# Performance work log

Measured on AMD Instinct MI355X. Metric: run time of the kernel, lower is better.

The kernel has to match this reference:

```python
import jax, jax.numpy as jnp
import numpy as np

# Multi-scale feature pyramid (static: determines per-level slice bounds)
SPATIAL_SHAPES = np.array([[100, 100], [50, 50], [25, 25], [13, 13], [7, 7]])  # (H, W) per level
LEVEL_START = np.concatenate([[0], np.cumsum(SPATIAL_SHAPES[:, 0] * SPATIAL_SHAPES[:, 1])])[:-1]
C = 256       # hidden_inplanes
HEADS = 8     # head_nums
POINTS = 4    # point_nums
LEVELS = 5    # feature_level_nums
FF = 2048     # feedforward_planes
DH = C // HEADS


def setup_inputs() -> dict:
    key = jax.random.key(0)
    ks = jax.random.split(key, 16)
    B = 2
    L = int((SPATIAL_SHAPES[:, 0] * SPATIAL_SHAPES[:, 1]).sum())  # 13343 tokens
    s = 0.02
    return {
        'src': jax.random.normal(ks[0], (B, L, C), jnp.float32),
        'pos': jax.random.normal(ks[1], (B, L, C), jnp.float32) * 0.1,
        'reference_points': jax.random.uniform(ks[2], (B, L, LEVELS, 2), jnp.float32),
        'wv': jax.random.normal(ks[3], (C, C), jnp.float32) * s,
        'bv': jnp.zeros((C,), jnp.float32),
        'wo': jax.random.normal(ks[4], (C, HEADS * LEVELS * POINTS * 2), jnp.float32) * s,
        'bo': jax.random.normal(ks[5], (HEADS * LEVELS * POINTS * 2,), jnp.float32) * 0.5,
        'wa': jax.random.normal(ks[6], (C, HEADS * LEVELS * POINTS), jnp.float32) * s,
        'ba': jnp.zeros((HEADS * LEVELS * POINTS,), jnp.float32),
        'wout': jax.random.normal(ks[7], (C, C), jnp.float32) * s,
        'bout': jnp.zeros((C,), jnp.float32),
        'ln1g': jnp.ones((C,), jnp.float32),
        'ln1b': jnp.zeros((C,), jnp.float32),
        'w1': jax.random.normal(ks[8], (C, FF), jnp.float32) * s,
        'b1': jnp.zeros((FF,), jnp.float32),
        'w2': jax.random.normal(ks[9], (FF, C), jnp.float32) * s,
        'b2': jnp.zeros((C,), jnp.float32),
        'ln2g': jnp.ones((C,), jnp.float32),
        'ln2b': jnp.zeros((C,), jnp.float32),
    }


def layernorm(x, g, b, eps=1e-5):
    m = jnp.mean(x, -1, keepdims=True)
    v = jnp.var(x, -1, keepdims=True)
    return (x - m) * jax.lax.rsqrt(v + eps) * g + b


def bilinear_sample(val, loc, Hs, Ws):
    # val: [B, heads, H*W, dh]   loc: [B, heads, Lq, P, 2] normalized coords in [0,1]
    # grid_sample semantics, align_corners=False, zero padding outside
    px = loc[..., 0] * Ws - 0.5
    py = loc[..., 1] * Hs - 0.5
    x0 = jnp.floor(px); y0 = jnp.floor(py)
    lx = px - x0;       ly = py - y0
    x0i = x0.astype(jnp.int32); y0i = y0.astype(jnp.int32)
    gather = jax.vmap(jax.vmap(lambda v, i: v[i]))  # over batch, head dims
    out = jnp.zeros(loc.shape[:-1] + (val.shape[-1],), val.dtype)
    for dx, dy, w in ((0, 0, (1 - lx) * (1 - ly)), (1, 0, lx * (1 - ly)),
                      (0, 1, (1 - lx) * ly), (1, 1, lx * ly)):
        xi = x0i + dx; yi = y0i + dy
        valid = (xi >= 0) & (xi < Ws) & (yi >= 0) & (yi < Hs)
        idx = jnp.clip(yi, 0, Hs - 1) * Ws + jnp.clip(xi, 0, Ws - 1)
        g = gather(val, idx)  # [B, heads, Lq, P, dh]
        out = out + (w * valid)[..., None] * g
    return out


def msdeform_attn(query, value_in, ref, wv, bv, wo, bo, wa, ba, wout, bout):
    B, Lq, _ = query.shape
    # value projection -> [B, heads, Len, dh]
    value = (value_in @ wv + bv).reshape(B, -1, HEADS, DH).transpose(0, 2, 1, 3)
    offsets = (query @ wo + bo).reshape(B, Lq, HEADS, LEVELS, POINTS, 2)
    attn = jax.nn.softmax((query @ wa + ba).reshape(B, Lq, HEADS, LEVELS * POINTS), -1)
    attn = attn.reshape(B, Lq, HEADS, LEVELS, POINTS)
    # offset normalizer = (W, H) per level
    norml = jnp.asarray(SPATIAL_SHAPES[:, ::-1].copy(), jnp.float32)
    loc = ref[:, :, None, :, None, :] + offsets / norml[None, None, None, :, None, :]
    acc = jnp.zeros((B, Lq, HEADS, DH), query.dtype)
    for l in range(LEVELS):
        Hs, Ws = int(SPATIAL_SHAPES[l, 0]), int(SPATIAL_SHAPES[l, 1])
        s = int(LEVEL_START[l])
        vl = value[:, :, s:s + Hs * Ws, :]
        locl = jnp.transpose(loc[:, :, :, l], (0, 2, 1, 3, 4))  # [B, heads, Lq, P, 2]
        samp = bilinear_sample(vl, locl, Hs, Ws)                 # [B, heads, Lq, P, dh]
        acc = acc + jnp.einsum('bhqpd,bqhp->bqhd', samp, attn[:, :, :, l])
    return acc.reshape(B, Lq, C) @ wout + bout


def reference(src, pos, reference_points, wv, bv, wo, bo, wa, ba, wout, bout,
              ln1g, ln1b, w1, b1, w2, b2, ln2g, ln2b):
    # DeformableTransformerEncoderLayer (eval mode, dropout off)
    q = src + pos
    src2 = msdeform_attn(q, src, reference_points, wv, bv, wo, bo, wa, ba, wout, bout)
    x = layernorm(src + src2, ln1g, ln1b)
    ffn = jax.nn.relu(x @ w1 + b1) @ w2 + b2
    return layernorm(x + ffn, ln2g, ln2b)
```

## Files before the change

### kernel.cpp

```cpp
#include <hip/hip_runtime.h>
#include <hip/hip_bf16.h>
#include <hip/hip_fp16.h>

typedef __hip_bfloat16 bf16;
typedef unsigned short ushort_t;
typedef __attribute__((ext_vector_type(8))) short bf16x8;
typedef __attribute__((ext_vector_type(16))) float f32x16;

__device__ __forceinline__ float us2f(unsigned short u) {
    unsigned int x = ((unsigned int)u) << 16;
    return __uint_as_float(x);
}
__device__ __forceinline__ ushort_t f2us(float f) {
    return ((__hip_bfloat16_raw)__float2bfloat16(f)).x;
}

__device__ __forceinline__ void gl_lds16(const ushort_t* g, ushort_t* l) {
    __builtin_amdgcn_global_load_lds(
        (const __attribute__((address_space(1))) void*)g,
        (__attribute__((address_space(3))) void*)l, 16, 0, 0);
}

__global__ __launch_bounds__(256) void cast2_kernel(
    const float* __restrict__ src, const float* __restrict__ pos,
    bf16* __restrict__ src_b, bf16* __restrict__ q_b, int n)
{
    int i = (blockIdx.x * 256 + threadIdx.x) * 4;
    if (i < n) {
        const float4 s4 = *reinterpret_cast<const float4*>(&src[i]);
        const float4 p4 = *reinterpret_cast<const float4*>(&pos[i]);
        int2 sp, qp;
        sp.x = (unsigned)f2us(s4.x) | ((unsigned)f2us(s4.y) << 16);
        sp.y = (unsigned)f2us(s4.z) | ((unsigned)f2us(s4.w) << 16);
        qp.x = (unsigned)f2us(s4.x + p4.x) | ((unsigned)f2us(s4.y + p4.y) << 16);
        qp.y = (unsigned)f2us(s4.z + p4.z) | ((unsigned)f2us(s4.w + p4.w) << 16);
        *reinterpret_cast<int2*>((ushort_t*)src_b + i) = sp;
        *reinterpret_cast<int2*>((ushort_t*)q_b + i) = qp;
    }
}

__global__ __launch_bounds__(256) void prep_kernel(
    const float* __restrict__ wv, const float* __restrict__ wo,
    const float* __restrict__ wa, const float* __restrict__ wout,
    const float* __restrict__ w1, const float* __restrict__ w2,
    const float* __restrict__ bo, const float* __restrict__ ba,
    bf16* __restrict__ wvt, bf16* __restrict__ wcat, bf16* __restrict__ woutt,
    bf16* __restrict__ w1t, bf16* __restrict__ w2t, float* __restrict__ bcat)
{
    __shared__ float tile[32][33];
    const int b = blockIdx.x;
    const float* W; bf16* Wt; int K, N, tb;
    if (b < 64)        { W = wv;   Wt = wvt;            K = 256;  N = 256;  tb = b; }
    else if (b < 144)  { W = wo;   Wt = wcat;           K = 256;  N = 320;  tb = b - 64; }
    else if (b < 184)  { W = wa;   Wt = wcat + 320*256; K = 256;  N = 160;  tb = b - 144; }
    else if (b < 248)  { W = wout; Wt = woutt;          K = 256;  N = 256;  tb = b - 184; }
    else if (b < 760)  { W = w1;   Wt = w1t;            K = 256;  N = 2048; tb = b - 248; }
    else if (b < 1272) { W = w2;   Wt = w2t;            K = 2048; N = 256;  tb = b - 760; }
    else {
        int i = (b - 1272) * 256 + threadIdx.x;
        if (i < 320) bcat[i] = bo[i];
        else if (i < 480) bcat[i] = ba[i - 320];
        return;
    }
    const int ntn = N >> 5;
    const int nb = (tb % ntn) * 32, kb = (tb / ntn) * 32;
    const int tx = threadIdx.x & 31, ty = threadIdx.x >> 5;
    #pragma unroll
    for (int i = 0; i < 32; i += 8) {
        int k = kb + ty + i, n = nb + tx;
        tile[ty + i][tx] = (k < K && n < N) ? W[(size_t)k * N + n] : 0.f;
    }
    __syncthreads();
    #pragma unroll
    for (int i = 0; i < 32; i += 8) {
        int n = nb + ty + i, k = kb + tx;
        if (n < N && k < K)
            Wt[(size_t)n * K + k] = __float2bfloat16(tile[tx][ty + i]);
    }
}

template<bool RELU, bool OUT_BF16, bool HAS_RESID, bool RESID_BF16, int NT, int WPE>
__global__ __launch_bounds__(256, WPE) void gemm_mfma_s(
    const ushort_t* __restrict__ A,
    const ushort_t* __restrict__ Bt,
    const float* __restrict__ bias,
    const void* __restrict__ residv,
    void* __restrict__ outv, int M, int N, int K, int mtiles)
{
    __shared__ __align__(16) char smemraw[24576];
    ushort_t* Asmem = (ushort_t*)smemraw;
    ushort_t* Bsmem = (ushort_t*)(smemraw + 4096);
    float (*epi)[68] = (float(*)[68])smemraw;

    const int lid = blockIdx.x;
    const int tbk = lid >> 3;
    const int xb = tbk & (NT - 1);
    const int yg = (tbk / NT) * 8 + (lid & 7);
    if (yg >= mtiles) return;
    const int m0 = yg * 64;
    const int n0 = xb * 128;

    const int tid = threadIdx.x;
    const int lane = tid & 63;
    const int wave = tid >> 6;
    const int l32 = lane & 31;
    const int hi  = lane >> 5;
    const int wm = wave >> 1;
    const int wn = wave & 1;

    const int lsup = lane >> 3;
    const int clin = lane & 7;

    const int gsA = wave * 8 + lsup;
    const int csA = clin ^ (gsA & 7);
    int rA = m0 + gsA * 2 + (csA >> 2); if (rA > M - 1) rA = M - 1;
    const ushort_t* aP = A + (size_t)rA * K + (csA & 3) * 8;
    ushort_t* aL = Asmem + wave * 512;

    const ushort_t* bP[2]; ushort_t* bL[2];
    #pragma unroll
    for (int i = 0; i < 2; ++i) {
        const int gsB = wave * 16 + i * 8 + lsup;
        const int csB = clin ^ (gsB & 7);
        int rB = n0 + gsB * 2 + (csB >> 2); if (rB > N - 1) rB = N - 1;
        bP[i] = Bt + (size_t)rB * K + (csB & 3) * 8;
        bL[i] = Bsmem + (wave * 16 + i * 8) * 64;
    }

    const int arow = wm * 32 + l32;
    const int asup = arow >> 1;
    const ushort_t* aR[2];
    #pragma unroll
    for (int kw = 0; kw < 2; ++kw) {
        const int q = kw * 2 + hi;
        const int slot = (((arow & 1) << 2) | q) ^ (asup & 7);
        aR[kw] = Asmem + asup * 64 + slot * 8;
    }
    const ushort_t* bR[2][2];
    #pragma unroll
    for (int j = 0; j < 2; ++j) {
        const int brow = wn * 64 + j * 32 + l32;
        const int bsup = brow >> 1;
        #pragma unroll
        for (int kw = 0; kw < 2; ++kw) {
            const int q = kw * 2 + hi;
            const int slot = (((brow & 1) << 2) | q) ^ (bsup & 7);
            bR[j][kw] = Bsmem + bsup * 64 + slot * 8;
        }
    }

    f32x16 acc[2] = {};

    auto stage = [&](int ofs) {
        gl_lds16(aP, aL + ofs);             aP    += 32;
        gl_lds16(bP[0], bL[0] + ofs);       bP[0] += 32;
        gl_lds16(bP[1], bL[1] + ofs);       bP[1] += 32;
    };
    auto compute = [&](int ofs) {
        #pragma unroll
        for (int kw = 0; kw < 2; ++kw) {
            const bf16x8 af = *reinterpret_cast<const bf16x8*>(aR[kw] + ofs);
            #pragma unroll
            for (int j = 0; j < 2; ++j)
                acc[j] = __builtin_amdgcn_mfma_f32_32x32x16_bf16(
                    af, *reinterpret_cast<const bf16x8*>(bR[j][kw] + ofs),
                    acc[j], 0, 0, 0);
        }
    };

    const int ntile = K >> 5;
    stage(0);
    for (int t = 0; t < ntile; t += 2) {
        __syncthreads();
        stage(6144);
        compute(0);
        __syncthreads();
        if (t + 2 < ntile) stage(0);
        compute(6144);
    }
    __syncthreads();

    #pragma unroll
    for (int half = 0; half < 2; ++half) {
        if (wn == half) {
            #pragma unroll
            for (int j = 0; j < 2; ++j) {
                const int coll = j * 32 + l32;
                const int n = n0 + half * 64 + coll;
                const float bv = (n < N) ? bias[n] : 0.f;
                #pragma unroll
                for (int r = 0; r < 16; ++r) {
                    const int row = wm * 32 + hi * 4 + (r & 3) + (r >> 2) * 8;
                    epi[row][coll] = acc[j][r] + bv;
                }
            }
        }
        __syncthreads();
        #pragma unroll
        for (int i = 0; i < 4; ++i) {
            const int idx = i * 256 + tid;
            const int row = idx >> 4;
            const int c4  = idx & 15;
            const int m = m0 + row;
            const int n = n0 + half * 64 + c4 * 4;
            if (m < M && n + 3 < N) {
                float4 v = *reinterpret_cast<const float4*>(&epi[row][c4 * 4]);
                if (HAS_RESID) {
                    if (RESID_BF16) {
                        const int2 rw = *reinterpret_cast<const int2*>(
                            (const ushort_t*)residv + (size_t)m * N + n);
                        v.x += us2f((ushort_t)((unsigned)rw.x & 0xffffu));
                        v.y += us2f((ushort_t)((unsigned)rw.x >> 16));
                        v.z += us2f((ushort_t)((unsigned)rw.y & 0xffffu));
                        v.w += us2f((ushort_t)((unsigned)rw.y >> 16));
                    } else {
                        const float4 r4 = *reinterpret_cast<const float4*>(
                            (const float*)residv + (size_t)m * N + n);
                        v.x += r4.x; v.y += r4.y; v.z += r4.z; v.w += r4.w;
                    }
                }
                if (RELU) {
                    v.x = fmaxf(v.x, 0.f); v.y = fmaxf(v.y, 0.f);
                    v.z = fmaxf(v.z, 0.f); v.w = fmaxf(v.w, 0.f);
                }
                if (OUT_BF16) {
                    int2 pk;
                    pk.x = (unsigned)f2us(v.x) | ((unsigned)f2us(v.y) << 16);
                    pk.y = (unsigned)f2us(v.z) | ((unsigned)f2us(v.w) << 16);
                    *reinterpret_cast<int2*>((ushort_t*)outv + (size_t)m * N + n) = pk;
                } else {
                    *reinterpret_cast<float4*>((float*)outv + (size_t)m * N + n) = v;
                }
            }
        }
        if (half == 0) __syncthreads();
    }
}

template<bool RELU, bool OUT_BF16, bool HAS_RESID, bool RESID_BF16, int NT>
__global__ __launch_bounds__(256, 4) void gemm_mfma_b(
    const ushort_t* __restrict__ A,
    const ushort_t* __restrict__ Bt,
    const float* __restrict__ bias,
    const void* __restrict__ residv,
    void* __restrict__ outv, int M, int N, int K, int mtiles)
{
    __shared__ __align__(16) char smemraw[32768];
    ushort_t* Asmem = (ushort_t*)smemraw;
    ushort_t* Bsmem = (ushort_t*)(smemraw + 8192);
    float (*epi)[68] = (float(*)[68])smemraw;

    const int lid = blockIdx.x;
    const int tbk = lid >> 3;
    const int xb = tbk & (NT - 1);
    const int yg = (tbk / NT) * 8 + (lid & 7);
    if (yg >= mtiles) return;
    const int m0 = yg * 128;
    const int n0 = xb * 128;

    const int tid = threadIdx.x;
    const int lane = tid & 63;
    const int wave = tid >> 6;
    const int l32 = lane & 31;
    const int hi  = lane >> 5;
    const int wm = wave >> 1;
    const int wn = wave & 1;

    const int lsup = lane >> 3;
    const int clin = lane & 7;
    const ushort_t *aP[2], *bP[2];
    ushort_t *aL[2], *bL[2];
    #pragma unroll
    for (int i = 0; i < 2; ++i) {
        const int gs = wave * 16 + i * 8 + lsup;
        const int cs = clin ^ (gs & 7);
        int rA = m0 + gs * 2 + (cs >> 2); if (rA > M - 1) rA = M - 1;
        aP[i] = A + (size_t)rA * K + (cs & 3) * 8;
        aL[i] = Asmem + (wave * 16 + i * 8) * 64;
        int rB = n0 + gs * 2 + (cs >> 2); if (rB > N - 1) rB = N - 1;
        bP[i] = Bt + (size_t)rB * K + (cs & 3) * 8;
        bL[i] = Bsmem + (wave * 16 + i * 8) * 64;
    }

    const ushort_t* aR[2][2];
    const ushort_t* bR[2][2];
    #pragma unroll
    for (int mi = 0; mi < 2; ++mi) {
        const int arow = wm * 64 + mi * 32 + l32;
        const int asup = arow >> 1;
        #pragma unroll
        for (int kw = 0; kw < 2; ++kw) {
            const int q = kw * 2 + hi;
            const int slot = (((arow & 1) << 2) | q) ^ (asup & 7);
            aR[mi][kw] = Asmem + asup * 64 + slot * 8;
        }
    }
    #pragma unroll
    for (int ni = 0; ni < 2; ++ni) {
        const int brow = wn * 64 + ni * 32 + l32;
        const int bsup = brow >> 1;
        #pragma unroll
        for (int kw = 0; kw < 2; ++kw) {
            const int q = kw * 2 + hi;
            const int slot = (((brow & 1) << 2) | q) ^ (bsup & 7);
            bR[ni][kw] = Bsmem + bsup * 64 + slot * 8;
        }
    }

    f32x16 a00 = {}, a01 = {}, a10 = {}, a11 = {};

    auto stage = [&](int ofs) {
        gl_lds16(aP[0], aL[0] + ofs); aP[0] += 32;
        gl_lds16(aP[1], aL[1] + ofs); aP[1] += 32;
        gl_lds16(bP[0], bL[0] + ofs); bP[0] += 32;
        gl_lds16(bP[1], bL[1] + ofs); bP[1] += 32;
    };
    auto compute = [&](int ofs) {
        #pragma unroll
        for (int kw = 0; kw < 2; ++kw) {
            const bf16x8 af0 = *reinterpret_cast<const bf16x8*>(aR[0][kw] + ofs);
            const bf16x8 af1 = *reinterpret_cast<const bf16x8*>(aR[1][kw] + ofs);
            const bf16x8 bf0 = *reinterpret_cast<const bf16x8*>(bR[0][kw] + ofs);
            const bf16x8 bf1 = *reinterpret_cast<const bf16x8*>(bR[1][kw] + ofs);
            a00 = __builtin_amdgcn_mfma_f32_32x32x16_bf16(af0, bf0, a00, 0, 0, 0);
            a01 = __builtin_amdgcn_mfma_f32_32x32x16_bf16(af0, bf1, a01, 0, 0, 0);
            a10 = __builtin_amdgcn_mfma_f32_32x32x16_bf16(af1, bf0, a10, 0, 0, 0);
            a11 = __builtin_amdgcn_mfma_f32_32x32x16_bf16(af1, bf1, a11, 0, 0, 0);
        }
    };

    const int ntile = K >> 5;
    stage(0);
    for (int t = 0; t < ntile; t += 2) {
        __syncthreads();
        stage(8192);
        compute(0);
        __syncthreads();
        if (t + 2 < ntile) stage(0);
        compute(8192);
    }
    __syncthreads();

    #pragma unroll
    for (int qd = 0; qd < 4; ++qd) {
        const int rh = qd >> 1, ch = qd & 1;
        if (qd) __syncthreads();
        if (wm == rh && wn == ch) {
            #pragma unroll
            for (int ni = 0; ni < 2; ++ni) {
                const int col = ni * 32 + l32;
                const int n = n0 + ch * 64 + col;
                const float bv = (n < N) ? bias[n] : 0.f;
                #pragma unroll
                for (int mi = 0; mi < 2; ++mi) {
                    const f32x16& ac = (mi == 0) ? (ni == 0 ? a00 : a01)
                                                 : (ni == 0 ? a10 : a11);
                    #pragma unroll
                    for (int r = 0; r < 16; ++r) {
                        const int row = mi * 32 + hi * 4 + (r & 3) + (r >> 2) * 8;
                        epi[row][col] = ac[r] + bv;
                    }
                }
            }
        }
        __syncthreads();
        #pragma unroll
        for (int i = 0; i < 4; ++i) {
            const int idx = i * 256 + tid;
            const int row = idx >> 4;
            const int c4  = idx & 15;
            const int m = m0 + rh * 64 + row;
            const int n = n0 + ch * 64 + c4 * 4;
            if (m < M && n + 3 < N) {
                float4 v = *reinterpret_cast<const float4*>(&epi[row][c4 * 4]);
                if (HAS_RESID) {
                    if (RESID_BF16) {
                        const int2 rw = *reinterpret_cast<const int2*>(
                            (const ushort_t*)residv + (size_t)m * N + n);
                        v.x += us2f((ushort_t)((unsigned)rw.x & 0xffffu));
                        v.y += us2f((ushort_t)((unsigned)rw.x >> 16));
                        v.z += us2f((ushort_t)((unsigned)rw.y & 0xffffu));
                        v.w += us2f((ushort_t)((unsigned)rw.y >> 16));
                    } else {
                        const float4 r4 = *reinterpret_cast<const float4*>(
                            (const float*)residv + (size_t)m * N + n);
                        v.x += r4.x; v.y += r4.y; v.z += r4.z; v.w += r4.w;
                    }
                }
                if (RELU) {
                    v.x = fmaxf(v.x, 0.f); v.y = fmaxf(v.y, 0.f);
                    v.z = fmaxf(v.z, 0.f); v.w = fmaxf(v.w, 0.f);
                }
                if (OUT_BF16) {
                    int2 pk;
                    pk.x = (unsigned)f2us(v.x) | ((unsigned)f2us(v.y) << 16);
                    pk.y = (unsigned)f2us(v.z) | ((unsigned)f2us(v.w) << 16);
                    *reinterpret_cast<int2*>((ushort_t*)outv + (size_t)m * N + n) = pk;
                } else {
                    *reinterpret_cast<float4*>((float*)outv + (size_t)m * N + n) = v;
                }
            }
        }
    }
}

__global__ __launch_bounds__(256) void msda_kernel_v7(
    const ushort_t* __restrict__ og,
    const float* __restrict__ refp,
    const ushort_t* __restrict__ value,
    bf16* __restrict__ out,
    int M, int L)
{
    const int tid = threadIdx.x;
    const int nb = gridDim.x;
    int wk = blockIdx.x;
    if ((nb & 7) == 0) {
        const int per = nb >> 3;
        wk = (blockIdx.x & 7) * per + (blockIdx.x >> 3);
    }
    const int qbase = wk * 8;

    __shared__ float s_attn[8][160];
    __shared__ int2  s_off[1280];
    __shared__ int2  s_wh[1280];

    for (int i = tid; i < 1280; i += 256) {
        int q = i / 160, j = i - q * 160;
        int qq = qbase + q;
        s_attn[q][j] = (qq < M) ? us2f(og[(size_t)qq * 480 + 320 + j]) : 0.f;
    }
    __syncthreads();

    if (tid < 64) {
        float* a = &s_attn[tid >> 3][(tid & 7) * 20];
        float mx = -1e30f;
        #pragma unroll
        for (int i = 0; i < 20; ++i) mx = fmaxf(mx, a[i]);
        float ssum = 0.f;
        #pragma unroll
        for (int i = 0; i < 20; ++i) {
            float e = __expf(a[i] - mx);
            a[i] = e;
            ssum += e;
        }
        float inv = 1.f / ssum;
        #pragma unroll
        for (int i = 0; i < 20; ++i) a[i] *= inv;
    }
    __syncthreads();

    #pragma unroll
    for (int it = 0; it < 5; ++it) {
        const int t = tid + it * 256;
        const int q  = t / 160;
        const int r  = t - q * 160;
        const int l  = (r - (r / 20) * 20) >> 2;
        const int qq = qbase + q;

        int2 offp = {0, 0};
        __half2 h01 = __floats2half2_rn(0.f, 0.f);
        __half2 h23 = h01;
        if (qq < M) {
            const int Wi = (l == 0) ? 100 : (l == 1) ? 50 : (l == 2) ? 25
                         : (l == 3) ? 13 : 7;
            const int s0 = (l == 0) ? 0 : (l == 1) ? 10000 : (l == 2) ? 12500
                         : (l == 3) ? 13125 : 13294;
            const float Wf = (float)Wi;
            const float ox = us2f(og[(size_t)qq * 480 + r * 2]);
            const float oy = us2f(og[(size_t)qq * 480 + r * 2 + 1]);
            const float2 rf = *reinterpret_cast<const float2*>(
                &refp[(size_t)qq * 10 + l * 2]);
            const float a = s_attn[q][r];

            const float px = fmaf(rf.x, Wf, -0.5f) + ox;
            const float py = fmaf(rf.y, Wf, -0.5f) + oy;
            const float x0f = floorf(px);
            const float y0f = floorf(py);
            const float lx = px - x0f;
            const float ly = py - y0f;
            const int x0 = (int)x0f;
            const int y0 = (int)y0f;

            const float wx0v = (x0 >= 0 && x0 < Wi) ? (1.f - lx) : 0.f;
            const float wx1v = (x0 + 1 >= 0 && x0 + 1 < Wi) ? lx : 0.f;
            const float wy0v = (y0 >= 0 && y0 < Wi) ? (1.f - ly) : 0.f;
            const float wy1v = (y0 + 1 >= 0 && y0 + 1 < Wi) ? ly : 0.f;

            const int c0 = min(max(x0, 0), Wi - 2);
            const int r0 = min(max(y0, 0), Wi - 2);
            const float swx0 = (x0 == c0 ? wx0v : 0.f) + (x0 + 1 == c0 ? wx1v : 0.f);
            const float swx1 = (x0 == c0 + 1 ? wx0v : 0.f) + (x0 + 1 == c0 + 1 ? wx1v : 0.f);
            const float swy0 = (y0 == r0 ? wy0v : 0.f) + (y0 + 1 == r0 ? wy1v : 0.f);
            const float swy1 = (y0 == r0 + 1 ? wy0v : 0.f) + (y0 + 1 == r0 + 1 ? wy1v : 0.f);

            offp.x = (s0 + r0 * Wi + c0) * 512;
            offp.y = offp.x + Wi * 512;
            h01 = __floats2half2_rn(a * swx0 * swy0, a * swx1 * swy0);
            h23 = __floats2half2_rn(a * swx0 * swy1, a * swx1 * swy1);
        }
        s_off[t] = offp;
        union { __half2 h; int i; } c0u, c1u;
        c0u.h = h01; c1u.h = h23;
        int2 wpk; wpk.x = c0u.i; wpk.y = c1u.i;
        s_wh[t] = wpk;
    }
    __syncthreads();

    const int qi  = tid >> 5;
    const int g   = tid & 31;
    const int h   = g >> 2;
    const int sub = g & 3;
    const int bq = qbase + qi;
    if (bq >= M) return;
    const int b = bq / L;

    const char* vb = (const char*)value + (size_t)b * L * 512 + h * 64 + sub * 16;

    float acc[8] = {};
    const int tb = qi * 160 + h * 20;
    #pragma unroll 2
    for (int p = 0; p < 20; ++p) {
        const int2 off = s_off[tb + p];
        const int2 whp = s_wh[tb + p];
        const int4 u00 = *reinterpret_cast<const int4*>(vb + off.x);
        const int4 u10 = *reinterpret_cast<const int4*>(vb + off.x + 512);
        const int4 u01 = *reinterpret_cast<const int4*>(vb + off.y);
        const int4 u11 = *reinterpret_cast<const int4*>(vb + off.y + 512);
        union { int i; __half2 h; } w0u, w1u;
        w0u.i = whp.x; w1u.i = whp.y;
        const float2 w01 = __half22float2(w0u.h);
        const float2 w23 = __half22float2(w1u.h);
        #define ACC4(u, wt)                                                        \
            acc[0] = fmaf(wt, __uint_as_float((unsigned)(u).x << 16), acc[0]);      \
            acc[1] = fmaf(wt, __uint_as_float((unsigned)(u).x & 0xffff0000u), acc[1]); \
            acc[2] = fmaf(wt, __uint_as_float((unsigned)(u).y << 16), acc[2]);      \
            acc[3] = fmaf(wt, __uint_as_float((unsigned)(u).y & 0xffff0000u), acc[3]); \
            acc[4] = fmaf(wt, __uint_as_float((unsigned)(u).z << 16), acc[4]);      \
            acc[5] = fmaf(wt, __uint_as_float((unsigned)(u).z & 0xffff0000u), acc[5]); \
            acc[6] = fmaf(wt, __uint_as_float((unsigned)(u).w << 16), acc[6]);      \
            acc[7] = fmaf(wt, __uint_as_float((unsigned)(u).w & 0xffff0000u), acc[7]);
        ACC4(u00, w01.x)
        ACC4(u10, w01.y)
        ACC4(u01, w23.x)
        ACC4(u11, w23.y)
        #undef ACC4
    }

    ushort_t o[8];
    #pragma unroll
    for (int i = 0; i < 8; ++i) o[i] = f2us(acc[i]);
    int4 pkt;
    pkt.x = (int)o[0] | ((int)o[1] << 16);
    pkt.y = (int)o[2] | ((int)o[3] << 16);
    pkt.z = (int)o[4] | ((int)o[5] << 16);
    pkt.w = (int)o[6] | ((int)o[7] << 16);
    *reinterpret_cast<int4*>((ushort_t*)out + (size_t)bq * 256 + h * 32 + sub * 8) = pkt;
}

template<bool OUT_BF16>
__global__ __launch_bounds__(256) void ln_kernel(
    const ushort_t* __restrict__ yb, const float* __restrict__ g,
    const float* __restrict__ bta, void* __restrict__ outv, int M)
{
    const int wave = threadIdx.x >> 6, lane = threadIdx.x & 63;
    const int row = blockIdx.x * 4 + wave;
    if (row >= M) return;
    const int2 raw = *reinterpret_cast<const int2*>(&yb[(size_t)row * 256 + lane * 4]);
    float v0 = us2f((ushort_t)((unsigned)raw.x & 0xffffu));
    float v1 = us2f((ushort_t)((unsigned)raw.x >> 16));
    float v2 = us2f((ushort_t)((unsigned)raw.y & 0xffffu));
    float v3 = us2f((ushort_t)((unsigned)raw.y >> 16));
    float s  = v0 + v1 + v2 + v3;
    float ss = v0 * v0 + v1 * v1 + v2 * v2 + v3 * v3;
    #pragma unroll
    for (int o = 32; o > 0; o >>= 1) {
        s += __shfl_down(s, o);
        ss += __shfl_down(ss, o);
    }
    s = __shfl(s, 0);
    ss = __shfl(ss, 0);
    const float mean = s * (1.f / 256.f);
    const float var = ss * (1.f / 256.f) - mean * mean;
    const float rs = rsqrtf(var + 1e-5f);
    const float4 g4 = *reinterpret_cast<const float4*>(&g[lane * 4]);
    const float4 b4 = *reinterpret_cast<const float4*>(&bta[lane * 4]);
    float4 o4;
    o4.x = (v0 - mean) * rs * g4.x + b4.x;
    o4.y = (v1 - mean) * rs * g4.y + b4.y;
    o4.z = (v2 - mean) * rs * g4.z + b4.z;
    o4.w = (v3 - mean) * rs * g4.w + b4.w;
    if (OUT_BF16) {
        int2 pk;
        pk.x = (unsigned)f2us(o4.x) | ((unsigned)f2us(o4.y) << 16);
        pk.y = (unsigned)f2us(o4.z) | ((unsigned)f2us(o4.w) << 16);
        *reinterpret_cast<int2*>((ushort_t*)outv + (size_t)row * 256 + lane * 4) = pk;
    } else {
        *reinterpret_cast<float4*>((float*)outv + (size_t)row * 256 + lane * 4) = o4;
    }
}

extern "C" void kernel_launch(void* const* d_in, const int* in_sizes, int n_in,
                              void* d_out, int out_size, void* d_ws, size_t ws_size,
                              hipStream_t stream)
{
    const int B = 2, L = 13343, C = 256, FF = 2048;
    const int M = B * L;

    const float* src  = (const float*)d_in[0];
    const float* pos  = (const float*)d_in[1];
    const float* refp = (const float*)d_in[2];
    const float* wv   = (const float*)d_in[3];
    const float* bv   = (const float*)d_in[4];
    const float* wo   = (const float*)d_in[5];
    const float* bo   = (const float*)d_in[6];
    const float* wa   = (const float*)d_in[7];
    const float* ba   = (const float*)d_in[8];
    const float* wout = (const float*)d_in[9];
    const float* bout = (const float*)d_in[10];
    const float* ln1g = (const float*)d_in[11];
    const float* ln1b = (const float*)d_in[12];
    const float* w1   = (const float*)d_in[13];
    const float* b1   = (const float*)d_in[14];
    const float* w2   = (const float*)d_in[15];
    const float* b2   = (const float*)d_in[16];
    const float* ln2g = (const float*)d_in[17];
    const float* ln2b = (const float*)d_in[18];

    char* ws = (char*)d_ws;
    const size_t MB = 1ull << 20;
    bf16*  src_b  = (bf16*)(ws + 0);
    bf16*  q_b    = (bf16*)(ws + 14 * MB);
    bf16*  val_b  = (bf16*)(ws + 28 * MB);
    bf16*  og     = (bf16*)(ws + 42 * MB);
    bf16*  acc_b  = (bf16*)(ws + 95 * MB);
    bf16*  h_b    = (bf16*)(ws + 0);
    bf16*  y      = (bf16*)(ws + 110 * MB);
    bf16*  z      = (bf16*)(ws + 110 * MB);
    bf16*  x_b    = (bf16*)(ws + 138 * MB);
    bf16* wvt    = (bf16*)(ws + 152 * MB);
    bf16* wcat   = wvt + 256 * 256;
    bf16* woutt  = wcat + 480 * 256;
    bf16* w1t    = woutt + 256 * 256;
    bf16* w2t    = w1t + 2048 * 256;
    float* bcat  = (float*)(w2t + 256 * 2048);
    (void)ws_size; (void)n_in; (void)in_sizes; (void)out_size;

    const int mt64  = (M + 63) / 64;
    const int gm8   = (mt64 + 7) / 8;
    const int mt128 = (M + 127) / 128;
    const int gb8   = (mt128 + 7) / 8;
    const int lnb   = (M + 3) / 4;

    prep_kernel<<<1274, 256, 0, stream>>>(wv, wo, wa, wout, w1, w2, bo, ba,
                                          wvt, wcat, woutt, w1t, w2t, bcat);

    cast2_kernel<<<(M * C / 4 + 255) / 256, 256, 0, stream>>>(
        src, pos, src_b, q_b, M * C);

    gemm_mfma_s<false, true, false, false, 2, 4><<<gm8 * 16, 256, 0, stream>>>(
        (const ushort_t*)src_b, (const ushort_t*)wvt, bv, nullptr, val_b,
        M, 256, 256, mt64);

    gemm_mfma_b<false, true, false, false, 4><<<gb8 * 32, 256, 0, stream>>>(
        (const ushort_t*)q_b, (const ushort_t*)wcat, bcat, nullptr, og,
        M, 480, 256, mt128);

    msda_kernel_v7<<<(M + 7) / 8, 256, 0, stream>>>(
        (const ushort_t*)og, refp, (const ushort_t*)val_b, acc_b, M, L);

    gemm_mfma_s<false, true, true, false, 2, 4><<<gm8 * 16, 256, 0, stream>>>(
        (const ushort_t*)acc_b, (const ushort_t*)woutt, bout, src, y,
        M, 256, 256, mt64);

    ln_kernel<true><<<lnb, 256, 0, stream>>>(
        (const ushort_t*)y, ln1g, ln1b, x_b, M);

    gemm_mfma_b<true, true, false, false, 16><<<gb8 * 128, 256, 0, stream>>>(
        (const ushort_t*)x_b, (const ushort_t*)w1t, b1, nullptr, h_b,
        M, FF, 256, mt128);

    gemm_mfma_b<false, true, true, true, 2><<<gb8 * 16, 256, 0, stream>>>(
        (const ushort_t*)h_b, (const ushort_t*)w2t, b2, x_b, z,
        M, 256, FF, mt128);

    ln_kernel<false><<<lnb, 256, 0, stream>>>(
        (const ushort_t*)z, ln2g, ln2b, (float*)d_out, M);
}
```

Before: 353.6 us.

## Fuse FFN up-projection, ReLU, down-projection and final LayerNorm into one kernel

Replaces the FF1 GEMM, the FF2 GEMM with residual, and the second LayerNorm with a single kernel. Each block holds a 64-row tile of x in LDS and loops over 16 chunks of 128 hidden units. It computes each ReLU hidden chunk into LDS and accumulates straight into the 256-wide output, then applies the residual and LayerNorm in the epilogue. This removes the large hidden-activation write and read to global memory and two launches. In exchange, weights are read directly from global memory without LDS staging, only about 417 blocks run, and there are barriers on every chunk.

```diff
diff --git a/kernel.cpp b/kernel.cpp
--- a/kernel.cpp
+++ b/kernel.cpp
@@ -399,6 +399,176 @@
                 } else {
                     *reinterpret_cast<float4*>((float*)outv + (size_t)m * N + n) = v;
                 }
+            }
+        }
+    }
+}
+
+__global__ __launch_bounds__(256, 2) void ffn_fused_kernel(
+    const ushort_t* __restrict__ X,
+    const ushort_t* __restrict__ W1t,
+    const ushort_t* __restrict__ W2t,
+    const float* __restrict__ b1, const float* __restrict__ b2,
+    const float* __restrict__ g, const float* __restrict__ beta,
+    float* __restrict__ out, int M, int mtiles)
+{
+    __shared__ __align__(16) char smem[49152];
+    ushort_t* Xs = (ushort_t*)smem;
+    ushort_t* Hs = (ushort_t*)(smem + 32768);
+    float (*epi)[260] = (float(*)[260])smem;
+
+    const int yg = blockIdx.x;
+    if (yg >= mtiles) return;
+    const int m0 = yg * 64;
+
+    const int tid = threadIdx.x;
+    const int lane = tid & 63;
+    const int wave = tid >> 6;
+    const int l32 = lane & 31;
+    const int hi  = lane >> 5;
+    const int wm  = wave >> 1;
+    const int wn  = wave & 1;
+
+    {
+        const int lsup = lane >> 3, clin = lane & 7;
+        const int gs = wave * 8 + lsup;
+        const int cs = clin ^ (gs & 7);
+        int r = m0 + gs * 2 + (cs >> 2); if (r > M - 1) r = M - 1;
+        const ushort_t* xp = X + (size_t)r * 256 + (cs & 3) * 8;
+        ushort_t* xl = Xs + wave * 512;
+        #pragma unroll
+        for (int t = 0; t < 8; ++t)
+            gl_lds16(xp + t * 32, xl + t * 2048);
+    }
+
+    const int arow = wm * 32 + l32;
+    const int asup = arow >> 1;
+    int aOff[2];
+    #pragma unroll
+    for (int kw = 0; kw < 2; ++kw) {
+        const int q = kw * 2 + hi;
+        const int slot = (((arow & 1) << 2) | q) ^ (asup & 7);
+        aOff[kw] = asup * 64 + slot * 8;
+    }
+    int hadr[16];
+    #pragma unroll
+    for (int r = 0; r < 16; ++r) {
+        const int row = wm * 32 + (r & 3) + 8 * (r >> 2) + 4 * hi;
+        const int slot = (((row & 1) << 2) | (l32 >> 3)) ^ ((row >> 1) & 7);
+        hadr[r] = (row >> 1) * 64 + slot * 8 + (l32 & 7);
+    }
+
+    const ushort_t* w1p = W1t + (size_t)(wn * 64 + l32) * 256 + hi * 8;
+    const ushort_t* w2p = W2t + (size_t)(wn * 128 + l32) * 2048 + hi * 8;
+
+    f32x16 za[4] = {};
+
+    __syncthreads();
+
+    for (int c = 0; c < 16; ++c) {
+        f32x16 h0 = {}, h1 = {};
+        const ushort_t* w1c = w1p + (size_t)c * 128 * 256;
+        #pragma unroll
+        for (int t = 0; t < 8; ++t) {
+            #pragma unroll
+            for (int kw = 0; kw < 2; ++kw) {
+                const bf16x8 af = *reinterpret_cast<const bf16x8*>(
+                    Xs + t * 2048 + aOff[kw]);
+                const bf16x8 bA = *reinterpret_cast<const bf16x8*>(
+                    w1c + t * 32 + kw * 16);
+                const bf16x8 bB = *reinterpret_cast<const bf16x8*>(
+                    w1c + 32 * 256 + t * 32 + kw * 16);
+                h0 = __builtin_amdgcn_mfma_f32_32x32x16_bf16(af, bA, h0, 0, 0, 0);
+                h1 = __builtin_amdgcn_mfma_f32_32x32x16_bf16(af, bB, h1, 0, 0, 0);
+            }
+        }
+        const float bb0 = b1[c * 128 + wn * 64 + l32];
+        const float bb1 = b1[c * 128 + wn * 64 + 32 + l32];
+
+        __syncthreads();
+        #pragma unroll
+        for (int r = 0; r < 16; ++r) {
+            Hs[(wn * 2 + 0) * 2048 + hadr[r]] = f2us(fmaxf(h0[r] + bb0, 0.f));
+            Hs[(wn * 2 + 1) * 2048 + hadr[r]] = f2us(fmaxf(h1[r] + bb1, 0.f));
+        }
+        __syncthreads();
+
+        const ushort_t* w2c = w2p + c * 128;
+        #pragma unroll
+        for (int t = 0; t < 4; ++t) {
+            #pragma unroll
+            for (int kw = 0; kw < 2; ++kw) {
+                const bf16x8 af = *reinterpret_cast<const bf16x8*>(
+                    Hs + t * 2048 + aOff[kw]);
+                #pragma unroll
+                for (int j = 0; j < 4; ++j) {
+                    const bf16x8 bf = *reinterpret_cast<const bf16x8*>(
+                        w2c + (size_t)j * 32 * 2048 + t * 32 + kw * 16);
+                    za[j] = __builtin_amdgcn_mfma_f32_32x32x16_bf16(
+                        af, bf, za[j], 0, 0, 0);
+                }
+            }
+        }
+    }
+
+    __syncthreads();
+
+    #pragma unroll
+    for (int p = 0; p < 2; ++p) {
+        if (p) __syncthreads();
+        if (wm == p) {
+            #pragma unroll
+            for (int j = 0; j < 4; ++j) {
+                const int col = wn * 128 + j * 32 + l32;
+                const float bz = b2[col];
+                #pragma unroll
+                for (int r = 0; r < 16; ++r) {
+                    const int row = (r & 3) + 8 * (r >> 2) + 4 * hi;
+                    epi[row][col] = za[j][r] + bz;
+                }
+            }
+        }
+        __syncthreads();
+        const int row = tid >> 3, t8 = tid & 7;
+        const int m = m0 + p * 32 + row;
+        const int mc = (m < M) ? m : (M - 1);
+        const ushort_t* xr = X + (size_t)mc * 256 + t8 * 32;
+        float v[32];
+        float s = 0.f, ss = 0.f;
+        #pragma unroll
+        for (int i = 0; i < 8; ++i) {
+            const float4 e = *reinterpret_cast<const float4*>(
+                &epi[row][t8 * 32 + i * 4]);
+            const int2 rb = *reinterpret_cast<const int2*>(xr + i * 4);
+            const float f0 = e.x + us2f((ushort_t)((unsigned)rb.x & 0xffffu));
+            const float f1 = e.y + us2f((ushort_t)((unsigned)rb.x >> 16));
+            const float f2 = e.z + us2f((ushort_t)((unsigned)rb.y & 0xffffu));
+            const float f3 = e.w + us2f((ushort_t)((unsigned)rb.y >> 16));
+            v[i * 4]     = f0; v[i * 4 + 1] = f1;
+            v[i * 4 + 2] = f2; v[i * 4 + 3] = f3;
+            s  += f0 + f1 + f2 + f3;
+            ss += f0 * f0 + f1 * f1 + f2 * f2 + f3 * f3;
+        }
+        s += __shfl_xor(s, 1); ss += __shfl_xor(ss, 1);
+        s += __shfl_xor(s, 2); ss += __shfl_xor(ss, 2);
+        s += __shfl_xor(s, 4); ss += __shfl_xor(ss, 4);
+        const float mean = s * (1.f / 256.f);
+        const float var = ss * (1.f / 256.f) - mean * mean;
+        const float rs = rsqrtf(var + 1e-5f);
+        if (m < M) {
+            #pragma unroll
+            for (int i = 0; i < 8; ++i) {
+                const float4 g4 = *reinterpret_cast<const float4*>(
+                    &g[t8 * 32 + i * 4]);
+                const float4 b4 = *reinterpret_cast<const float4*>(
+                    &beta[t8 * 32 + i * 4]);
+                float4 o4;
+                o4.x = (v[i * 4]     - mean) * rs * g4.x + b4.x;
+                o4.y = (v[i * 4 + 1] - mean) * rs * g4.y + b4.y;
+                o4.z = (v[i * 4 + 2] - mean) * rs * g4.z + b4.z;
+                o4.w = (v[i * 4 + 3] - mean) * rs * g4.w + b4.w;
+                *reinterpret_cast<float4*>(
+                    &out[(size_t)m * 256 + t8 * 32 + i * 4]) = o4;
             }
         }
     }
@@ -633,9 +803,7 @@
     bf16*  val_b  = (bf16*)(ws + 28 * MB);
     bf16*  og     = (bf16*)(ws + 42 * MB);
     bf16*  acc_b  = (bf16*)(ws + 95 * MB);
-    bf16*  h_b    = (bf16*)(ws + 0);
     bf16*  y      = (bf16*)(ws + 110 * MB);
-    bf16*  z      = (bf16*)(ws + 110 * MB);
     bf16*  x_b    = (bf16*)(ws + 138 * MB);
     bf16* wvt    = (bf16*)(ws + 152 * MB);
     bf16* wcat   = wvt + 256 * 256;
@@ -675,14 +843,7 @@
     ln_kernel<true><<<lnb, 256, 0, stream>>>(
         (const ushort_t*)y, ln1g, ln1b, x_b, M);
 
-    gemm_mfma_b<true, true, false, false, 16><<<gb8 * 128, 256, 0, stream>>>(
-        (const ushort_t*)x_b, (const ushort_t*)w1t, b1, nullptr, h_b,
-        M, FF, 256, mt128);
-
-    gemm_mfma_b<false, true, true, true, 2><<<gb8 * 16, 256, 0, stream>>>(
-        (const ushort_t*)h_b, (const ushort_t*)w2t, b2, x_b, z,
-        M, 256, FF, mt128);
-
-    ln_kernel<false><<<lnb, 256, 0, stream>>>(
-        (const ushort_t*)z, ln2g, ln2b, (float*)d_out, M);
-}
+    ffn_fused_kernel<<<mt64, 256, 0, stream>>>(
+        (const ushort_t*)x_b, (const ushort_t*)w1t, (const ushort_t*)w2t,
+        b1, b2, ln2g, ln2b, (float*)d_out, M, mt64);
+}
```

Result: slower. 496.3 us (+40.3%).
